# Performance work log

Measured on AMD Instinct MI355X. Metric: run time of the kernel, lower is better.

## Reference

```python
import jax, jax.numpy as jnp
import numpy as np
from math import pi, sqrt, factorial

NUM_SPHERICAL = 7
NUM_RADIAL = 6
CUTOFF = 5.0


def _sph_jn_np(x, n):
    # spherical Bessel j_n(x) in float64 numpy via upward recurrence
    x = np.asarray(x, dtype=np.float64)
    jm = np.sin(x) / x
    if n == 0:
        return jm
    jc = np.sin(x) / x**2 - np.cos(x) / x
    for l in range(2, n + 1):
        jm, jc = jc, (2 * l - 1) / x * jc - jm
    return jc


def _jn_zeros(n, k):
    # first k positive zeros of j_l for l = 0..n-1 (zeros of j_l interleave those of j_{l-1})
    nz = k + n
    z = np.zeros((n, nz))
    z[0] = np.arange(1, nz + 1) * np.pi
    for l in range(1, n):
        for j in range(nz - l):
            a, b = z[l - 1, j], z[l - 1, j + 1]
            fa = _sph_jn_np(a, l)
            for _ in range(100):
                m = 0.5 * (a + b)
                fm = _sph_jn_np(m, l)
                if fa * fm <= 0:
                    b = m
                else:
                    a, fa = m, fm
            z[l, j] = 0.5 * (a + b)
    return z[:, :k]


_ZEROS_NP = _jn_zeros(NUM_SPHERICAL, NUM_RADIAL)  # (n, k)
_NORM_NP = np.array([[(0.5 * _sph_jn_np(_ZEROS_NP[l, j], l + 1) ** 2) ** -0.5
                      for j in range(NUM_RADIAL)] for l in range(NUM_SPHERICAL)])
BESSEL_ZEROS = jnp.asarray(_ZEROS_NP, dtype=jnp.float32)  # z_{l,j}
BESSEL_NORM = jnp.asarray(_NORM_NP, dtype=jnp.float32)    # sqrt(2)/|j_{l+1}(z_{l,j})|


def _rbf(dist):
    # normalized spherical Bessel basis: rbf[:, l*k + j] = norm[l,j] * j_l(z_{l,j} * dist/cutoff)
    d = dist / CUTOFF
    u = d[:, None, None] * BESSEL_ZEROS[None]  # (E, n, k)
    cols = []
    for l in range(NUM_SPHERICAL):
        x = u[:, l, :]
        jm = jnp.sin(x) / x  # j_0
        if l == 0:
            jc = jm
        else:
            jc = jnp.sin(x) / (x * x) - jnp.cos(x) / x  # j_1
        for ll in range(2, l + 1):
            jm, jc = jc, (2 * ll - 1) / x * jc - jm
        cols.append(BESSEL_NORM[l] * jc)
    return jnp.concatenate(cols, axis=1)  # (E, n*k)


def _cbf(angle, phi):
    # real spherical harmonics Y_{l,m}(angle, phi), flat order m = -l..l per l
    n = NUM_SPHERICAL
    z = jnp.cos(angle)
    s = jnp.sin(angle)
    P = {(0, 0): jnp.ones_like(z)}
    for m in range(1, n):
        P[(m, m)] = (1 - 2 * m) * s * P[(m - 1, m - 1)]  # Condon-Shortley phase included
    for m in range(0, n - 1):
        P[(m + 1, m)] = (2 * m + 1) * z * P[(m, m)]
    for m in range(n):
        for l in range(m + 2, n):
            P[(l, m)] = ((2 * l - 1) * z * P[(l - 1, m)] - (l + m - 1) * P[(l - 2, m)]) / (l - m)

    def pref(l, m):
        return sqrt((2 * l + 1) * factorial(l - m) / (4.0 * pi * factorial(l + m)))

    cols = [jnp.full_like(angle, 0.5 / sqrt(pi))]  # Y_00 constant
    for l in range(1, n):
        for m in range(-l, l + 1):
            am = abs(m)
            if m < 0:
                cols.append(sqrt(2.0) * pref(l, am) * jnp.sin(am * phi) * P[(l, am)])
            elif m == 0:
                cols.append(pref(l, 0) * P[(l, 0)])
            else:
                cols.append(sqrt(2.0) * pref(l, am) * jnp.cos(am * phi) * P[(l, am)])
    return jnp.stack(cols, axis=1)  # (T, n*n)


def setup_inputs() -> dict:
    key = jax.random.key(0)
    kd, ka, kp, ki = jax.random.split(key, 4)
    E, T = 150000, 500000
    dist = jax.random.uniform(kd, (E,), minval=0.5, maxval=5.0, dtype=jnp.float32)
    angle = jax.random.uniform(ka, (T,), minval=0.0, maxval=float(np.pi), dtype=jnp.float32)
    phi = jax.random.uniform(kp, (T,), minval=-float(np.pi), maxval=float(np.pi), dtype=jnp.float32)
    idx_kj = jax.random.randint(ki, (T,), 0, E)
    return {"dist": dist, "angle": angle, "phi": phi, "idx_kj": idx_kj}


def reference(dist, angle, phi, idx_kj):
    n, k = NUM_SPHERICAL, NUM_RADIAL
    rbf = _rbf(dist)          # (E, n*k)
    cbf = _cbf(angle, phi)    # (T, n*n)
    out = (rbf[idx_kj].reshape(-1, 1, n, k) * cbf.reshape(-1, n, n, 1)).reshape(-1, n * n * k)
    return out
```

## Files before the change

### kernel.cpp

```cpp
#include <hip/hip_runtime.h>
#include <math.h>

#ifndef M_PI
#define M_PI 3.14159265358979323846
#endif

#define NS 7
#define NK 6
#define GT 64
#define BT 256
#define NC (NS*NS)
#define NR (NS*NK)
#define NF2 147

typedef float f32x2 __attribute__((ext_vector_type(2)));
typedef float f32x4 __attribute__((ext_vector_type(4)));


__device__ void jl_pair(double x, int l, double& jl, double& jm1) {
  double s = sin(x), c = cos(x);
  double j0 = s / x;
  double jm = c / x;
  if (l == 0) { jl = j0; jm1 = jm; return; }
  double j1 = (s / x - c) / x;
  for (int ll = 2; ll <= l; ++ll) {
    double t = (2.0 * ll - 1.0) / x * j1 - j0;
    j0 = j1; j1 = t;
  }
  jl = j1; jm1 = j0;
}

__global__ void setup_kernel(float* tab) {
  int id = threadIdx.x;
  if (id < NS * NK) {
    int l = id / NK, j = id % NK;
    double nu = l + 0.5;
    double mu = 4.0 * nu * nu;
    double b  = ((double)(j + 1) + 0.5 * nu - 0.25) * M_PI;
    double b8 = 8.0 * b;
    double x = b - (mu - 1.0) / b8
                 - 4.0 * (mu - 1.0) * (7.0 * mu - 31.0) / (3.0 * b8 * b8 * b8)
                 - 32.0 * (mu - 1.0) * (83.0 * mu * mu - 982.0 * mu + 3779.0) /
                   (15.0 * b8 * b8 * b8 * b8 * b8);
    double jl, jm1;
    for (int it = 0; it < 4; ++it) {
      jl_pair(x, l, jl, jm1);
      double dj = jm1 - (l + 1.0) / x * jl;
      x -= jl / dj;
    }
    tab[id] = (float)x;
    jl_pair(x, l, jl, jm1);
    double jp1 = (2.0 * l + 1.0) / x * jl - jm1;
    tab[NS * NK + id] = (float)(sqrt(2.0) / fabs(jp1));
  }
  if (id >= 64 && id < 64 + NC) {
    int c = id - 64;
    double v;
    if (c == 0) {
      v = 0.5 / sqrt(M_PI);
    } else {
      int l = 1;
      while ((l + 1) * (l + 1) <= c) ++l;
      int m  = c - l * l - l;
      int am = m < 0 ? -m : m;
      double fr = 1.0;
      for (int i2 = l - am + 1; i2 <= l + am; ++i2) fr *= (double)i2;
      double pref = sqrt((2.0 * l + 1.0) / (4.0 * M_PI * fr));
      v = (m != 0) ? sqrt(2.0) * pref : pref;
    }
    tab[2 * NS * NK + c] = (float)v;
  }
}

__global__ __launch_bounds__(BT, 4) void torsion_kernel(
    const float* __restrict__ dist, const float* __restrict__ angle,
    const float* __restrict__ phi, const int* __restrict__ idx_kj,
    const float* __restrict__ tab, float* __restrict__ out, int T) {
  __shared__ float s_cbf[GT][NC];
  __shared__ __align__(16) float s_rbf[GT][NR];
  __shared__ float s_d[GT];
  __shared__ float s_tab[133];
  __shared__ unsigned short s_map[NF2 + 1];

  const int tid = threadIdx.x;
  const int t0  = blockIdx.x * GT;
  const int nt  = min(GT, T - t0);

  float a = 0.0f, ph = 0.0f;
  if (tid < GT) {
    int t = t0 + tid;
    float dd = 1.0f;
    if (t < T) {
      dd = dist[idx_kj[t]] * 0.2f;
      a  = angle[t];
      ph = phi[t];
    }
    s_d[tid] = dd;
  }
  if (tid < 133) s_tab[tid] = tab[tid];
  if (tid < NF2) {
    int ii = tid / 21, rem2 = tid - 21 * ii, jj = rem2 / 3;
    s_map[tid] = (unsigned short)((ii * NS + jj) | (rem2 << 8));
  }
  __syncthreads();

  if (tid < GT) {
    if (t0 + tid < T) {
      float z = cosf(a), s = sinf(a);
      float sp, cp;
      sincosf(ph, &sp, &cp);
      float cmv[NS], smv[NS];
      cmv[0] = 1.0f; smv[0] = 0.0f;
      cmv[1] = cp;   smv[1] = sp;
#pragma unroll
      for (int m = 2; m < NS; ++m) {
        cmv[m] = 2.0f * cp * cmv[m - 1] - cmv[m - 2];
        smv[m] = 2.0f * cp * smv[m - 1] - smv[m - 2];
      }
      const float* coef = s_tab + 2 * NR;
      float* crow = s_cbf[tid];
      float pmm = 1.0f;
#pragma unroll
      for (int m = 0; m < NS; ++m) {
        float pl1 = pmm, pl2 = 0.0f;
#pragma unroll
        for (int l = m; l < NS; ++l) {
          float plm;
          if (l == m)          plm = pmm;
          else if (l == m + 1) plm = (float)(2 * m + 1) * z * pmm;
          else                 plm = ((float)(2 * l - 1) * z * pl1 -
                                      (float)(l + m - 1) * pl2) *
                                     (float)(1.0 / (double)(l - m));
          int cpn = l * l + l + m;
          if (m == 0) {
            crow[cpn] = coef[cpn] * plm;
          } else {
            crow[cpn] = coef[cpn] * cmv[m] * plm;
            crow[l * l + l - m] = coef[l * l + l - m] * smv[m] * plm;
          }
          pl2 = pl1; pl1 = plm;
        }
        pmm = (float)(-1 - 2 * m) * s * pmm;
      }
    }
  } else {
    int j  = tid - 64;
    int t  = j / NR;
    int cc = j - NR * t;
    int i2 = j;
    float* rlin = &s_rbf[0][0];
#pragma unroll 2
    for (int it = 0; it < 14; ++it) {
      int l = (cc * 43) >> 8;
      float x = s_d[t] * s_tab[cc];
      float sx, cx;
      sincosf(x, &sx, &cx);
      float invx = 1.0f / x;
      float jm = sx * invx;
      float jc;
      if (l == 0) jc = jm;
      else {
        jc = (sx * invx - cx) * invx;
#pragma unroll
        for (int ll = 2; ll <= 6; ++ll) {
          if (ll <= l) {
            float tt = (float)(2 * ll - 1) * invx * jc - jm;
            jm = jc; jc = tt;
          }
        }
      }
      rlin[i2] = s_tab[NR + cc] * jc;
      i2 += 192;
      cc += 24; t += 4;
      if (cc >= NR) { cc -= NR; ++t; }
    }
  }
  __syncthreads();

  const f32x2* r2 = (const f32x2*)&s_rbf[0][0];

  auto body = [&](int i, int p, int k, f32x4* o4) {
    int t2 = p << 1;
    int c2 = k << 1;
    int toff0 = (c2 >= NF2) ? 1 : 0;
    int cc0 = c2 - (toff0 ? NF2 : 0);
    int ta = t2 + toff0;
    unsigned mp0 = s_map[cc0];
    float cv0 = s_cbf[ta][mp0 & 0xff];
    f32x2 rv0 = r2[ta * 21 + (mp0 >> 8)];
    int c21 = c2 + 1;
    int toff1 = (c21 >= NF2) ? 1 : 0;
    int cc1 = c21 - (toff1 ? NF2 : 0);
    int tb = t2 + toff1;
    unsigned mp1 = s_map[cc1];
    float cv1 = s_cbf[tb][mp1 & 0xff];
    f32x2 rv1 = r2[tb * 21 + (mp1 >> 8)];
    f32x4 ov = {cv0 * rv0.x, cv0 * rv0.y, cv1 * rv1.x, cv1 * rv1.y};
    __builtin_nontemporal_store(ov, o4 + i);
  };

  if (nt == GT) {
    f32x4* o4 = (f32x4*)out + (size_t)blockIdx.x * 4704;
    int i = tid, p = 0, k = tid;
    if (k >= NF2) { k -= NF2; p = 1; }
#pragma unroll 3
    for (int it = 0; it < 18; ++it) {
      body(i, p, k, o4);
      i += BT; k += 109; ++p;
      if (k >= NF2) { k -= NF2; ++p; }
    }
    if (tid < 96) body(i, p, k, o4);
  } else {
    f32x2* o2 = (f32x2*)out + (size_t)t0 * NF2;
    int tot = nt * NF2;
    for (int i = tid; i < tot; i += BT) {
      int t  = i / NF2;
      int c2 = i - NF2 * t;
      unsigned mp = s_map[c2];
      float cv = s_cbf[t][mp & 0xff];
      f32x2 rv = r2[t * 21 + (mp >> 8)];
      f32x2 ov = cv * rv;
      __builtin_nontemporal_store(ov, o2 + i);
    }
  }
}

extern "C" void kernel_launch(void* const* d_in, const int* in_sizes, int n_in,
                              void* d_out, int out_size, void* d_ws, size_t ws_size,
                              hipStream_t stream) {
  const float* dist  = (const float*)d_in[0];
  const float* angle = (const float*)d_in[1];
  const float* phi   = (const float*)d_in[2];
  const int*   idx   = (const int*)d_in[3];
  float* out = (float*)d_out;
  float* tab = (float*)d_ws;
  int T = in_sizes[1];

  hipLaunchKernelGGL(setup_kernel, dim3(1), dim3(128), 0, stream, tab);
  int nb = (T + GT - 1) / GT;
  hipLaunchKernelGGL(torsion_kernel, dim3(nb), dim3(BT), 0, stream,
                     dist, angle, phi, idx, tab, out, T);
}
```

Baseline: 128.0 us.

## Precompute per-edge RBF table once and gather it in the torsion kernel

Adds a kernel that evaluates the spherical Bessel basis once per edge (E entries) into a workspace table, and the main kernel now gathers 42-float rows by idx_kj instead of recomputing the RBF per triplet (T > E). The setup kernel also moves the Bessel zero search to float with an extra Newton step. This removes redundant transcendental work but adds an extra launch, writing and reading the table in global memory, and random gathers. It falls back to the old path when the workspace is too small.

```diff
diff --git a/kernel.cpp b/kernel.cpp
--- a/kernel.cpp
+++ b/kernel.cpp
@@ -17,14 +17,15 @@
 typedef float f32x4 __attribute__((ext_vector_type(4)));
 
 
-__device__ void jl_pair(double x, int l, double& jl, double& jm1) {
-  double s = sin(x), c = cos(x);
-  double j0 = s / x;
-  double jm = c / x;
+__device__ void jl_pair_f(float x, int l, float& jl, float& jm1) {
+  float s, c;
+  __sincosf(x, &s, &c);
+  float invx = 1.0f / x;
+  float j0 = s * invx, jm = c * invx;
   if (l == 0) { jl = j0; jm1 = jm; return; }
-  double j1 = (s / x - c) / x;
+  float j1 = (s * invx - c) * invx;
   for (int ll = 2; ll <= l; ++ll) {
-    double t = (2.0 * ll - 1.0) / x * j1 - j0;
+    float t = (2.0f * ll - 1.0f) * invx * j1 - j0;
     j0 = j1; j1 = t;
   }
   jl = j1; jm1 = j0;
@@ -34,52 +35,80 @@
   int id = threadIdx.x;
   if (id < NS * NK) {
     int l = id / NK, j = id % NK;
-    double nu = l + 0.5;
-    double mu = 4.0 * nu * nu;
-    double b  = ((double)(j + 1) + 0.5 * nu - 0.25) * M_PI;
-    double b8 = 8.0 * b;
-    double x = b - (mu - 1.0) / b8
-                 - 4.0 * (mu - 1.0) * (7.0 * mu - 31.0) / (3.0 * b8 * b8 * b8)
-                 - 32.0 * (mu - 1.0) * (83.0 * mu * mu - 982.0 * mu + 3779.0) /
-                   (15.0 * b8 * b8 * b8 * b8 * b8);
-    double jl, jm1;
-    for (int it = 0; it < 4; ++it) {
-      jl_pair(x, l, jl, jm1);
-      double dj = jm1 - (l + 1.0) / x * jl;
+    float nu = l + 0.5f, mu = 4.0f * nu * nu;
+    float b  = ((float)(j + 1) + 0.5f * nu - 0.25f) * (float)M_PI;
+    float b8 = 8.0f * b;
+    float x = b - (mu - 1.0f) / b8
+                - 4.0f * (mu - 1.0f) * (7.0f * mu - 31.0f) / (3.0f * b8 * b8 * b8)
+                - 32.0f * (mu - 1.0f) * (83.0f * mu * mu - 982.0f * mu + 3779.0f) /
+                  (15.0f * b8 * b8 * b8 * b8 * b8);
+    float jl, jm1;
+    for (int it = 0; it < 5; ++it) {
+      jl_pair_f(x, l, jl, jm1);
+      float dj = jm1 - (l + 1.0f) / x * jl;
       x -= jl / dj;
     }
-    tab[id] = (float)x;
-    jl_pair(x, l, jl, jm1);
-    double jp1 = (2.0 * l + 1.0) / x * jl - jm1;
-    tab[NS * NK + id] = (float)(sqrt(2.0) / fabs(jp1));
-  }
-  if (id >= 64 && id < 64 + NC) {
-    int c = id - 64;
+    tab[id] = x;
+    jl_pair_f(x, l, jl, jm1);
+    float jp1 = (2.0f * l + 1.0f) / x * jl - jm1;
+    tab[NS * NK + id] = sqrtf(2.0f) / fabsf(jp1);
+  }
+  if (id < NC) {
     double v;
-    if (c == 0) {
+    if (id == 0) {
       v = 0.5 / sqrt(M_PI);
     } else {
       int l = 1;
-      while ((l + 1) * (l + 1) <= c) ++l;
-      int m  = c - l * l - l;
+      while ((l + 1) * (l + 1) <= id) ++l;
+      int m  = id - l * l - l;
       int am = m < 0 ? -m : m;
       double fr = 1.0;
       for (int i2 = l - am + 1; i2 <= l + am; ++i2) fr *= (double)i2;
       double pref = sqrt((2.0 * l + 1.0) / (4.0 * M_PI * fr));
       v = (m != 0) ? sqrt(2.0) * pref : pref;
     }
-    tab[2 * NS * NK + c] = (float)v;
-  }
-}
-
-__global__ __launch_bounds__(BT, 4) void torsion_kernel(
-    const float* __restrict__ dist, const float* __restrict__ angle,
-    const float* __restrict__ phi, const int* __restrict__ idx_kj,
-    const float* __restrict__ tab, float* __restrict__ out, int T) {
+    tab[2 * NS * NK + id] = (float)v;
+  }
+}
+
+__global__ __launch_bounds__(256) void rbf_table_kernel(
+    const float* __restrict__ dist, const float* __restrict__ tab,
+    float* __restrict__ table, int E) {
+  int tloc = threadIdx.x;
+  if (tloc >= 252) return;
+  int eloc = (tloc * 1561) >> 16;
+  int cc   = tloc - 42 * eloc;
+  int e    = blockIdx.x * 6 + eloc;
+  if (e >= E) return;
+  int l = (cc * 43) >> 8;
+  float x = dist[e] * 0.2f * tab[cc];
+  float sx, cx;
+  __sincosf(x, &sx, &cx);
+  float invx = 1.0f / x;
+  float jm = sx * invx;
+  float jc;
+  if (l == 0) jc = jm;
+  else {
+    jc = (sx * invx - cx) * invx;
+#pragma unroll
+    for (int ll = 2; ll <= 6; ++ll) {
+      if (ll <= l) {
+        float tt = (float)(2 * ll - 1) * invx * jc - jm;
+        jm = jc; jc = tt;
+      }
+    }
+  }
+  table[(size_t)e * NR + cc] = tab[NR + cc] * jc;
+}
+
+__global__ __launch_bounds__(BT, 4) void torsion_gather_kernel(
+    const float* __restrict__ angle, const float* __restrict__ phi,
+    const int* __restrict__ idx_kj, const float* __restrict__ tab,
+    const float* __restrict__ table, float* __restrict__ out, int T) {
   __shared__ float s_cbf[GT][NC];
-  __shared__ __align__(16) float s_rbf[GT][NR];
-  __shared__ float s_d[GT];
-  __shared__ float s_tab[133];
+  __shared__ __align__(8) float s_rbf[GT][NR];
+  __shared__ int s_e[GT];
+  __shared__ float s_coef[NC];
   __shared__ unsigned short s_map[NF2 + 1];
 
   const int tid = threadIdx.x;
@@ -89,15 +118,15 @@
   float a = 0.0f, ph = 0.0f;
   if (tid < GT) {
     int t = t0 + tid;
-    float dd = 1.0f;
+    int e = 0;
     if (t < T) {
-      dd = dist[idx_kj[t]] * 0.2f;
+      e  = idx_kj[t];
       a  = angle[t];
       ph = phi[t];
     }
-    s_d[tid] = dd;
-  }
-  if (tid < 133) s_tab[tid] = tab[tid];
+    s_e[tid] = e;
+  }
+  if (tid >= 64 && tid < 64 + NC) s_coef[tid - 64] = tab[2 * NR + (tid - 64)];
   if (tid < NF2) {
     int ii = tid / 21, rem2 = tid - 21 * ii, jj = rem2 / 3;
     s_map[tid] = (unsigned short)((ii * NS + jj) | (rem2 << 8));
@@ -117,7 +146,6 @@
         cmv[m] = 2.0f * cp * cmv[m - 1] - cmv[m - 2];
         smv[m] = 2.0f * cp * smv[m - 1] - smv[m - 2];
       }
-      const float* coef = s_tab + 2 * NR;
       float* crow = s_cbf[tid];
       float pmm = 1.0f;
 #pragma unroll
@@ -133,10 +161,10 @@
                                      (float)(1.0 / (double)(l - m));
           int cpn = l * l + l + m;
           if (m == 0) {
-            crow[cpn] = coef[cpn] * plm;
+            crow[cpn] = s_coef[cpn] * plm;
           } else {
-            crow[cpn] = coef[cpn] * cmv[m] * plm;
-            crow[l * l + l - m] = coef[l * l + l - m] * smv[m] * plm;
+            crow[cpn] = s_coef[cpn] * cmv[m] * plm;
+            crow[l * l + l - m] = s_coef[l * l + l - m] * smv[m] * plm;
           }
           pl2 = pl1; pl1 = plm;
         }
@@ -144,35 +172,17 @@
       }
     }
   } else {
-    int j  = tid - 64;
-    int t  = j / NR;
-    int cc = j - NR * t;
-    int i2 = j;
-    float* rlin = &s_rbf[0][0];
-#pragma unroll 2
-    for (int it = 0; it < 14; ++it) {
-      int l = (cc * 43) >> 8;
-      float x = s_d[t] * s_tab[cc];
-      float sx, cx;
-      sincosf(x, &sx, &cx);
-      float invx = 1.0f / x;
-      float jm = sx * invx;
-      float jc;
-      if (l == 0) jc = jm;
-      else {
-        jc = (sx * invx - cx) * invx;
-#pragma unroll
-        for (int ll = 2; ll <= 6; ++ll) {
-          if (ll <= l) {
-            float tt = (float)(2 * ll - 1) * invx * jc - jm;
-            jm = jc; jc = tt;
-          }
-        }
-      }
-      rlin[i2] = s_tab[NR + cc] * jc;
-      i2 += 192;
-      cc += 24; t += 4;
-      if (cc >= NR) { cc -= NR; ++t; }
+    int j2  = tid - 64;
+    int t   = (j2 * 3121) >> 16;
+    int rem = j2 - 21 * t;
+    f32x2* rl = (f32x2*)&s_rbf[0][0];
+#pragma unroll
+    for (int it = 0; it < 7; ++it) {
+      const f32x2* src = (const f32x2*)table + (size_t)s_e[t] * 21 + rem;
+      rl[j2] = *src;
+      j2 += 192;
+      rem += 3; t += 9;
+      if (rem >= 21) { rem -= 21; ++t; }
     }
   }
   __syncthreads();
@@ -225,6 +235,159 @@
   }
 }
 
+__global__ __launch_bounds__(BT, 4) void torsion_kernel(
+    const float* __restrict__ dist, const float* __restrict__ angle,
+    const float* __restrict__ phi, const int* __restrict__ idx_kj,
+    const float* __restrict__ tab, float* __restrict__ out, int T) {
+  __shared__ float s_cbf[GT][NC];
+  __shared__ __align__(16) float s_rbf[GT][NR];
+  __shared__ float s_d[GT];
+  __shared__ float s_tab[133];
+  __shared__ unsigned short s_map[NF2 + 1];
+
+  const int tid = threadIdx.x;
+  const int t0  = blockIdx.x * GT;
+  const int nt  = min(GT, T - t0);
+
+  float a = 0.0f, ph = 0.0f;
+  if (tid < GT) {
+    int t = t0 + tid;
+    float dd = 1.0f;
+    if (t < T) {
+      dd = dist[idx_kj[t]] * 0.2f;
+      a  = angle[t];
+      ph = phi[t];
+    }
+    s_d[tid] = dd;
+  }
+  if (tid < 133) s_tab[tid] = tab[tid];
+  if (tid < NF2) {
+    int ii = tid / 21, rem2 = tid - 21 * ii, jj = rem2 / 3;
+    s_map[tid] = (unsigned short)((ii * NS + jj) | (rem2 << 8));
+  }
+  __syncthreads();
+
+  if (tid < GT) {
+    if (t0 + tid < T) {
+      float z = cosf(a), s = sinf(a);
+      float sp, cp;
+      sincosf(ph, &sp, &cp);
+      float cmv[NS], smv[NS];
+      cmv[0] = 1.0f; smv[0] = 0.0f;
+      cmv[1] = cp;   smv[1] = sp;
+#pragma unroll
+      for (int m = 2; m < NS; ++m) {
+        cmv[m] = 2.0f * cp * cmv[m - 1] - cmv[m - 2];
+        smv[m] = 2.0f * cp * smv[m - 1] - smv[m - 2];
+      }
+      const float* coef = s_tab + 2 * NR;
+      float* crow = s_cbf[tid];
+      float pmm = 1.0f;
+#pragma unroll
+      for (int m = 0; m < NS; ++m) {
+        float pl1 = pmm, pl2 = 0.0f;
+#pragma unroll
+        for (int l = m; l < NS; ++l) {
+          float plm;
+          if (l == m)          plm = pmm;
+          else if (l == m + 1) plm = (float)(2 * m + 1) * z * pmm;
+          else                 plm = ((float)(2 * l - 1) * z * pl1 -
+                                      (float)(l + m - 1) * pl2) *
+                                     (float)(1.0 / (double)(l - m));
+          int cpn = l * l + l + m;
+          if (m == 0) {
+            crow[cpn] = coef[cpn] * plm;
+          } else {
+            crow[cpn] = coef[cpn] * cmv[m] * plm;
+            crow[l * l + l - m] = coef[l * l + l - m] * smv[m] * plm;
+          }
+          pl2 = pl1; pl1 = plm;
+        }
+        pmm = (float)(-1 - 2 * m) * s * pmm;
+      }
+    }
+  } else {
+    int j  = tid - 64;
+    int t  = j / NR;
+    int cc = j - NR * t;
+    int i2 = j;
+    float* rlin = &s_rbf[0][0];
+#pragma unroll 2
+    for (int it = 0; it < 14; ++it) {
+      int l = (cc * 43) >> 8;
+      float x = s_d[t] * s_tab[cc];
+      float sx, cx;
+      sincosf(x, &sx, &cx);
+      float invx = 1.0f / x;
+      float jm = sx * invx;
+      float jc;
+      if (l == 0) jc = jm;
+      else {
+        jc = (sx * invx - cx) * invx;
+#pragma unroll
+        for (int ll = 2; ll <= 6; ++ll) {
+          if (ll <= l) {
+            float tt = (float)(2 * ll - 1) * invx * jc - jm;
+            jm = jc; jc = tt;
+          }
+        }
+      }
+      rlin[i2] = s_tab[NR + cc] * jc;
+      i2 += 192;
+      cc += 24; t += 4;
+      if (cc >= NR) { cc -= NR; ++t; }
+    }
+  }
+  __syncthreads();
+
+  const f32x2* r2 = (const f32x2*)&s_rbf[0][0];
+
+  auto body = [&](int i, int p, int k, f32x4* o4) {
+    int t2 = p << 1;
+    int c2 = k << 1;
+    int toff0 = (c2 >= NF2) ? 1 : 0;
+    int cc0 = c2 - (toff0 ? NF2 : 0);
+    int ta = t2 + toff0;
+    unsigned mp0 = s_map[cc0];
+    float cv0 = s_cbf[ta][mp0 & 0xff];
+    f32x2 rv0 = r2[ta * 21 + (mp0 >> 8)];
+    int c21 = c2 + 1;
+    int toff1 = (c21 >= NF2) ? 1 : 0;
+    int cc1 = c21 - (toff1 ? NF2 : 0);
+    int tb = t2 + toff1;
+    unsigned mp1 = s_map[cc1];
+    float cv1 = s_cbf[tb][mp1 & 0xff];
+    f32x2 rv1 = r2[tb * 21 + (mp1 >> 8)];
+    f32x4 ov = {cv0 * rv0.x, cv0 * rv0.y, cv1 * rv1.x, cv1 * rv1.y};
+    __builtin_nontemporal_store(ov, o4 + i);
+  };
+
+  if (nt == GT) {
+    f32x4* o4 = (f32x4*)out + (size_t)blockIdx.x * 4704;
+    int i = tid, p = 0, k = tid;
+    if (k >= NF2) { k -= NF2; p = 1; }
+#pragma unroll 3
+    for (int it = 0; it < 18; ++it) {
+      body(i, p, k, o4);
+      i += BT; k += 109; ++p;
+      if (k >= NF2) { k -= NF2; ++p; }
+    }
+    if (tid < 96) body(i, p, k, o4);
+  } else {
+    f32x2* o2 = (f32x2*)out + (size_t)t0 * NF2;
+    int tot = nt * NF2;
+    for (int i = tid; i < tot; i += BT) {
+      int t  = i / NF2;
+      int c2 = i - NF2 * t;
+      unsigned mp = s_map[c2];
+      float cv = s_cbf[t][mp & 0xff];
+      f32x2 rv = r2[t * 21 + (mp >> 8)];
+      f32x2 ov = cv * rv;
+      __builtin_nontemporal_store(ov, o2 + i);
+    }
+  }
+}
+
 extern "C" void kernel_launch(void* const* d_in, const int* in_sizes, int n_in,
                               void* d_out, int out_size, void* d_ws, size_t ws_size,
                               hipStream_t stream) {
@@ -234,10 +397,21 @@
   const int*   idx   = (const int*)d_in[3];
   float* out = (float*)d_out;
   float* tab = (float*)d_ws;
+  int E = in_sizes[0];
   int T = in_sizes[1];
-
-  hipLaunchKernelGGL(setup_kernel, dim3(1), dim3(128), 0, stream, tab);
   int nb = (T + GT - 1) / GT;
-  hipLaunchKernelGGL(torsion_kernel, dim3(nb), dim3(BT), 0, stream,
-                     dist, angle, phi, idx, tab, out, T);
-}
+
+  hipLaunchKernelGGL(setup_kernel, dim3(1), dim3(64), 0, stream, tab);
+
+  size_t need = 1024 + (size_t)E * NR * sizeof(float);
+  if (ws_size >= need) {
+    float* table = (float*)((char*)d_ws + 1024);
+    hipLaunchKernelGGL(rbf_table_kernel, dim3((E + 5) / 6), dim3(256), 0, stream,
+                       dist, tab, table, E);
+    hipLaunchKernelGGL(torsion_gather_kernel, dim3(nb), dim3(BT), 0, stream,
+                       angle, phi, idx, tab, table, out, T);
+  } else {
+    hipLaunchKernelGGL(torsion_kernel, dim3(nb), dim3(BT), 0, stream,
+                       dist, angle, phi, idx, tab, out, T);
+  }
+}
```

After: 136.6 us. 6.7% more time.

## Software-pipeline output gather loop and switch setup kernel to float math

Applied to the files above, without the earlier changes.

The output loop is restructured. All 18 map entries are preloaded into registers, and each entry now packs two column mappings, so one LDS read serves both output pairs. The LDS gathers for the next two iterations are issued ahead of the multiply and nontemporal store of the current one. The setup kernel's Bessel zero Newton solve moves from double to single precision with fast sincos, and the launch shrinks to 64 threads. This cuts FP64 latency in the serial setup kernel but risks lower precision in the Bessel zeros and norms, and adds register pressure from the preload.

```diff
diff --git a/kernel.cpp b/kernel.cpp
--- a/kernel.cpp
+++ b/kernel.cpp
@@ -17,14 +17,15 @@
 typedef float f32x4 __attribute__((ext_vector_type(4)));
 
 
-__device__ void jl_pair(double x, int l, double& jl, double& jm1) {
-  double s = sin(x), c = cos(x);
-  double j0 = s / x;
-  double jm = c / x;
+__device__ void jl_pair_f(float x, int l, float& jl, float& jm1) {
+  float s, c;
+  __sincosf(x, &s, &c);
+  float invx = 1.0f / x;
+  float j0 = s * invx, jm = c * invx;
   if (l == 0) { jl = j0; jm1 = jm; return; }
-  double j1 = (s / x - c) / x;
+  float j1 = (s * invx - c) * invx;
   for (int ll = 2; ll <= l; ++ll) {
-    double t = (2.0 * ll - 1.0) / x * j1 - j0;
+    float t = (2.0f * ll - 1.0f) * invx * j1 - j0;
     j0 = j1; j1 = t;
   }
   jl = j1; jm1 = j0;
@@ -34,41 +35,39 @@
   int id = threadIdx.x;
   if (id < NS * NK) {
     int l = id / NK, j = id % NK;
-    double nu = l + 0.5;
-    double mu = 4.0 * nu * nu;
-    double b  = ((double)(j + 1) + 0.5 * nu - 0.25) * M_PI;
-    double b8 = 8.0 * b;
-    double x = b - (mu - 1.0) / b8
-                 - 4.0 * (mu - 1.0) * (7.0 * mu - 31.0) / (3.0 * b8 * b8 * b8)
-                 - 32.0 * (mu - 1.0) * (83.0 * mu * mu - 982.0 * mu + 3779.0) /
-                   (15.0 * b8 * b8 * b8 * b8 * b8);
-    double jl, jm1;
-    for (int it = 0; it < 4; ++it) {
-      jl_pair(x, l, jl, jm1);
-      double dj = jm1 - (l + 1.0) / x * jl;
+    float nu = l + 0.5f, mu = 4.0f * nu * nu;
+    float b  = ((float)(j + 1) + 0.5f * nu - 0.25f) * (float)M_PI;
+    float b8 = 8.0f * b;
+    float x = b - (mu - 1.0f) / b8
+                - 4.0f * (mu - 1.0f) * (7.0f * mu - 31.0f) / (3.0f * b8 * b8 * b8)
+                - 32.0f * (mu - 1.0f) * (83.0f * mu * mu - 982.0f * mu + 3779.0f) /
+                  (15.0f * b8 * b8 * b8 * b8 * b8);
+    float jl, jm1;
+    for (int it = 0; it < 5; ++it) {
+      jl_pair_f(x, l, jl, jm1);
+      float dj = jm1 - (l + 1.0f) / x * jl;
       x -= jl / dj;
     }
-    tab[id] = (float)x;
-    jl_pair(x, l, jl, jm1);
-    double jp1 = (2.0 * l + 1.0) / x * jl - jm1;
-    tab[NS * NK + id] = (float)(sqrt(2.0) / fabs(jp1));
-  }
-  if (id >= 64 && id < 64 + NC) {
-    int c = id - 64;
+    tab[id] = x;
+    jl_pair_f(x, l, jl, jm1);
+    float jp1 = (2.0f * l + 1.0f) / x * jl - jm1;
+    tab[NS * NK + id] = sqrtf(2.0f) / fabsf(jp1);
+  }
+  if (id < NC) {
     double v;
-    if (c == 0) {
+    if (id == 0) {
       v = 0.5 / sqrt(M_PI);
     } else {
       int l = 1;
-      while ((l + 1) * (l + 1) <= c) ++l;
-      int m  = c - l * l - l;
+      while ((l + 1) * (l + 1) <= id) ++l;
+      int m  = id - l * l - l;
       int am = m < 0 ? -m : m;
       double fr = 1.0;
       for (int i2 = l - am + 1; i2 <= l + am; ++i2) fr *= (double)i2;
       double pref = sqrt((2.0 * l + 1.0) / (4.0 * M_PI * fr));
       v = (m != 0) ? sqrt(2.0) * pref : pref;
     }
-    tab[2 * NS * NK + c] = (float)v;
+    tab[2 * NS * NK + id] = (float)v;
   }
 }
 
@@ -77,10 +76,10 @@
     const float* __restrict__ phi, const int* __restrict__ idx_kj,
     const float* __restrict__ tab, float* __restrict__ out, int T) {
   __shared__ float s_cbf[GT][NC];
-  __shared__ __align__(16) float s_rbf[GT][NR];
+  __shared__ __align__(8) float s_rbf[GT][NR];
   __shared__ float s_d[GT];
   __shared__ float s_tab[133];
-  __shared__ unsigned short s_map[NF2 + 1];
+  __shared__ unsigned s_map2[NF2];
 
   const int tid = threadIdx.x;
   const int t0  = blockIdx.x * GT;
@@ -99,8 +98,14 @@
   }
   if (tid < 133) s_tab[tid] = tab[tid];
   if (tid < NF2) {
-    int ii = tid / 21, rem2 = tid - 21 * ii, jj = rem2 / 3;
-    s_map[tid] = (unsigned short)((ii * NS + jj) | (rem2 << 8));
+    auto mk = [](int cc) {
+      int ii = (cc * 3121) >> 16;
+      int rem2 = cc - 21 * ii;
+      int jj = (rem2 * 86) >> 8;
+      return (unsigned)((ii * NS + jj) | (rem2 << 8));
+    };
+    int cc1 = tid + 1; if (cc1 == NF2) cc1 = 0;
+    s_map2[tid] = mk(tid) | (mk(cc1) << 16);
   }
   __syncthreads();
 
@@ -179,45 +184,75 @@
 
   const f32x2* r2 = (const f32x2*)&s_rbf[0][0];
 
-  auto body = [&](int i, int p, int k, f32x4* o4) {
-    int t2 = p << 1;
-    int c2 = k << 1;
-    int toff0 = (c2 >= NF2) ? 1 : 0;
-    int cc0 = c2 - (toff0 ? NF2 : 0);
-    int ta = t2 + toff0;
-    unsigned mp0 = s_map[cc0];
-    float cv0 = s_cbf[ta][mp0 & 0xff];
-    f32x2 rv0 = r2[ta * 21 + (mp0 >> 8)];
-    int c21 = c2 + 1;
-    int toff1 = (c21 >= NF2) ? 1 : 0;
-    int cc1 = c21 - (toff1 ? NF2 : 0);
-    int tb = t2 + toff1;
-    unsigned mp1 = s_map[cc1];
-    float cv1 = s_cbf[tb][mp1 & 0xff];
-    f32x2 rv1 = r2[tb * 21 + (mp1 >> 8)];
-    f32x4 ov = {cv0 * rv0.x, cv0 * rv0.y, cv1 * rv1.x, cv1 * rv1.y};
-    __builtin_nontemporal_store(ov, o4 + i);
-  };
-
   if (nt == GT) {
-    f32x4* o4 = (f32x4*)out + (size_t)blockIdx.x * 4704;
-    int i = tid, p = 0, k = tid;
+    f32x4* o4 = (f32x4*)out + (size_t)blockIdx.x * 4704 + tid;
+
+    int k = tid, p = 0;
     if (k >= NF2) { k -= NF2; p = 1; }
-#pragma unroll 3
+
+    unsigned m[18];
+    {
+      int cc = k << 1; if (cc >= NF2) cc -= NF2;
+#pragma unroll
+      for (int it = 0; it < 18; ++it) {
+        m[it] = s_map2[cc];
+        cc += 71; if (cc >= NF2) cc -= NF2;
+      }
+    }
+
+    float cva[3], cvb[3];
+    f32x2 rva[3], rvb[3];
+    int ki = k, pi = p;
+
+    auto ISSUE = [&](int slot, int it) {
+      int t2 = pi << 1;
+      int ta = t2 + (ki >= 74 ? 1 : 0);
+      int tb = t2 + (ki >= 73 ? 1 : 0);
+      unsigned mp = m[it];
+      unsigned i0 = mp & 0xffu,          r0 = (mp >> 8) & 0xffu;
+      unsigned i1 = (mp >> 16) & 0xffu,  r1 = mp >> 24;
+      cva[slot] = s_cbf[ta][i0];
+      rva[slot] = r2[ta * 21 + r0];
+      cvb[slot] = s_cbf[tb][i1];
+      rvb[slot] = r2[tb * 21 + r1];
+      ki += 109; ++pi;
+      if (ki >= NF2) { ki -= NF2; ++pi; }
+    };
+
+    ISSUE(0, 0);
+    ISSUE(1, 1);
+#pragma unroll
     for (int it = 0; it < 18; ++it) {
-      body(i, p, k, o4);
-      i += BT; k += 109; ++p;
-      if (k >= NF2) { k -= NF2; ++p; }
-    }
-    if (tid < 96) body(i, p, k, o4);
+      if (it + 2 < 18) ISSUE((it + 2) % 3, it + 2);
+      int sl = it % 3;
+      f32x4 ov = {cva[sl] * rva[sl].x, cva[sl] * rva[sl].y,
+                  cvb[sl] * rvb[sl].x, cvb[sl] * rvb[sl].y};
+      __builtin_nontemporal_store(ov, o4 + it * 256);
+    }
+
+    if (tid < 96) {
+      int cc = ki << 1; if (cc >= NF2) cc -= NF2;
+      unsigned mp = s_map2[cc];
+      int t2 = pi << 1;
+      int ta = t2 + (ki >= 74 ? 1 : 0);
+      int tb = t2 + (ki >= 73 ? 1 : 0);
+      unsigned i0 = mp & 0xffu,          r0 = (mp >> 8) & 0xffu;
+      unsigned i1 = (mp >> 16) & 0xffu,  r1 = mp >> 24;
+      float cv0 = s_cbf[ta][i0];
+      f32x2 rv0 = r2[ta * 21 + r0];
+      float cv1 = s_cbf[tb][i1];
+      f32x2 rv1 = r2[tb * 21 + r1];
+      f32x4 ov = {cv0 * rv0.x, cv0 * rv0.y, cv1 * rv1.x, cv1 * rv1.y};
+      __builtin_nontemporal_store(ov, o4 + 18 * 256);
+    }
   } else {
     f32x2* o2 = (f32x2*)out + (size_t)t0 * NF2;
     int tot = nt * NF2;
     for (int i = tid; i < tot; i += BT) {
       int t  = i / NF2;
       int c2 = i - NF2 * t;
-      unsigned mp = s_map[c2];
-      float cv = s_cbf[t][mp & 0xff];
+      unsigned mp = s_map2[c2] & 0xffffu;
+      float cv = s_cbf[t][mp & 0xffu];
       f32x2 rv = r2[t * 21 + (mp >> 8)];
       f32x2 ov = cv * rv;
       __builtin_nontemporal_store(ov, o2 + i);
@@ -236,7 +271,7 @@
   float* tab = (float*)d_ws;
   int T = in_sizes[1];
 
-  hipLaunchKernelGGL(setup_kernel, dim3(1), dim3(128), 0, stream, tab);
+  hipLaunchKernelGGL(setup_kernel, dim3(1), dim3(64), 0, stream, tab);
   int nb = (T + GT - 1) / GT;
   hipLaunchKernelGGL(torsion_kernel, dim3(nb), dim3(BT), 0, stream,
                      dist, angle, phi, idx, tab, out, T);
```

After: 127.2 us. About the same (-0.6%).
